# Performance work log

Measured on AMD Instinct MI355X. Metric: run time of the kernel, lower is better.

## Reference

```python
import jax, jax.numpy as jnp
import numpy as np

B, NC, H, W = 8, 384, 32, 32
G, GC = 6, 64            # n_groups, n_group_channels
HEADS, D = 12, 32        # n_heads, n_head_channels
KS, STRIDE = 3, 2
ORF = 2.0                # offset_range_factor
HK = (H - KS) // STRIDE + 1
WK = (W - KS) // STRIDE + 1
NS = HK * WK             # n_sample per branch
NQ = H * W               # query length


def setup_inputs() -> dict:
    key = jax.random.key(0)
    ks = jax.random.split(key, 16)
    def n(k, shape, s=0.02):
        return jax.random.normal(k, shape, jnp.float32) * s
    return {
        "query": jax.random.normal(ks[0], (B, NC, 1, NQ), jnp.float32),
        "x_r1": jax.random.normal(ks[1], (B, NC, H, W), jnp.float32),
        "x_r2": jax.random.normal(ks[2], (B, NC, H, W), jnp.float32),
        "x_x1": jax.random.normal(ks[3], (B, NC, H, W), jnp.float32),
        "x_x2": jax.random.normal(ks[4], (B, NC, H, W), jnp.float32),
        # conv_offset: 1x1 (4gc->gc) + GELU + depthwise kk stride + GELU + 1x1 (gc->2, no bias)
        "off_w1": n(ks[5], (GC, 4 * GC)),
        "off_b1": jnp.zeros((GC,), jnp.float32),
        "off_w2": n(ks[6], (GC, 1, KS, KS), 0.1),
        "off_b2": jnp.zeros((GC,), jnp.float32),
        "off_w3": n(ks[7], (2, GC), 0.1),
        "q_w": n(ks[8], (NC, NC)), "q_b": jnp.zeros((NC,), jnp.float32),
        "k_w": n(ks[9], (NC, NC)), "k_b": jnp.zeros((NC,), jnp.float32),
        "v_w": n(ks[10], (NC, NC)), "v_b": jnp.zeros((NC,), jnp.float32),
        "o_w": n(ks[11], (NC, NC)), "o_b": jnp.zeros((NC,), jnp.float32),
    }


def _conv1x1(x, w, b=None):
    # x: (B, Cin, ...), w: (Cout, Cin)
    y = jnp.einsum('oc,bc...->bo...', w, x)
    if b is not None:
        y = y + b.reshape((1, -1) + (1,) * (y.ndim - 2))
    return y


def _forward(query, x_r1, x_r2, x_x1, x_x2, off_w1, off_b1, off_w2, off_b2,
             off_w3, q_w, q_b, k_w, k_b, v_w, v_b, o_w, o_b):
    gelu = lambda t: jax.nn.gelu(t, approximate=False)
    # shared offset branch: concat 4 maps along channels, split into groups
    data = jnp.concatenate([x_r1, x_r2, x_x1, x_x2], axis=1).reshape(B * G, 4 * GC, H, W)
    t = gelu(_conv1x1(data, off_w1, off_b1))
    t = jax.lax.conv_general_dilated(
        t, off_w2, (STRIDE, STRIDE), 'VALID',
        feature_group_count=GC,
        dimension_numbers=('NCHW', 'OIHW', 'NCHW')) + off_b2[None, :, None, None]
    t = gelu(t)
    offset = _conv1x1(t, off_w3)                      # (BG, 2, HK, WK), ch0=y, ch1=x
    orange = jnp.array([1.0 / (HK - 1.0), 1.0 / (WK - 1.0)], jnp.float32).reshape(1, 2, 1, 1)
    offset = jnp.tanh(offset) * orange * ORF
    offset = offset.transpose(0, 2, 3, 1)             # (BG, HK, WK, 2)
    # reference points (normalized to [-1,1], align_corners=True convention)
    cy = (jnp.arange(HK, dtype=jnp.float32) * STRIDE + KS // 2) / (H - 1.0) * 2.0 - 1.0
    cx = (jnp.arange(WK, dtype=jnp.float32) * STRIDE + KS // 2) / (W - 1.0) * 2.0 - 1.0
    ref = jnp.stack(jnp.meshgrid(cy, cx, indexing='ij'), axis=-1)  # (HK, WK, 2)
    pos = jnp.clip(offset + ref[None], -1.0, 1.0).reshape(B * G, NS, 2)
    gy, gx = pos[..., 0], pos[..., 1]
    # bilinear grid sample, align_corners=True; grid clamped so always in-bounds
    x = (gx + 1.0) * 0.5 * (W - 1)
    y = (gy + 1.0) * 0.5 * (H - 1)
    x0f, y0f = jnp.floor(x), jnp.floor(y)
    wx = (x - x0f)[:, None, :]
    wy = (y - y0f)[:, None, :]
    x0 = jnp.clip(x0f.astype(jnp.int32), 0, W - 1); x1 = jnp.clip(x0 + 1, 0, W - 1)
    y0 = jnp.clip(y0f.astype(jnp.int32), 0, H - 1); y1 = jnp.clip(y0 + 1, 0, H - 1)

    def bsample(img):
        flat = img.reshape(B * G, GC, H * W)
        gat = lambda yi, xi: jnp.take_along_axis(flat, (yi * W + xi)[:, None, :], axis=2)
        out = (gat(y0, x0) * (1 - wy) * (1 - wx) + gat(y0, x1) * (1 - wy) * wx +
               gat(y1, x0) * wy * (1 - wx) + gat(y1, x1) * wy * wx)
        return out.reshape(B, NC, NS)

    sampled = jnp.concatenate(
        [bsample(x_r1), bsample(x_r2), bsample(x_x1), bsample(x_x2)], axis=-1)  # (B, NC, 4*NS)
    q = _conv1x1(query.reshape(B, NC, NQ), q_w, q_b).reshape(B * HEADS, D, NQ)
    k = _conv1x1(sampled, k_w, k_b).reshape(B * HEADS, D, 4 * NS)
    v = _conv1x1(sampled, v_w, v_b).reshape(B * HEADS, D, 4 * NS)
    attn = jax.nn.softmax(jnp.einsum('bcm,bcn->bmn', q, k) * (D ** -0.5), axis=-1)
    out = jnp.einsum('bmn,bcn->bcm', attn, v).reshape(B, NC, NQ)
    out = _conv1x1(out, o_w, o_b)
    return query.reshape(B, NC, NQ) + out  # == out.squeeze(2) of torch


def reference(query, x_r1, x_r2, x_x1, x_x2, off_w1, off_b1, off_w2, off_b2,
              off_w3, q_w, q_b, k_w, k_b, v_w, v_b, o_w, o_b):
    return _forward(query, x_r1, x_r2, x_x1, x_x2, off_w1, off_b1, off_w2,
                    off_b2, off_w3, q_w, q_b, k_w, k_b, v_w, v_b, o_w, o_b)
```

## Files before the change

### kernel.cpp

```cpp
#include <hip/hip_runtime.h>
#include <math.h>

#define Bn 8
#define NCn 384
#define Hn 32
#define Wn 32
#define Gn 6
#define GCn 64
#define HEADSn 12
#define Dn 32
#define HKn 15
#define WKn 15
#define NSn 225
#define NQn 1024
#define NKVn 900
#define VSTRIDE 960

typedef __attribute__((ext_vector_type(8))) short short8;
typedef __attribute__((ext_vector_type(4))) float floatx4;

__device__ __forceinline__ float gelu_f(float x) {
    return 0.5f * x * (1.0f + erff(x * 0.70710678118654752f));
}

__device__ __forceinline__ ushort f2bf(float x) {
    unsigned u = __float_as_uint(x);
    u = (u + 0x7FFF + ((u >> 16) & 1)) >> 16;
    return (ushort)u;
}

__device__ __forceinline__ ushort f2bf_fast(float x) {
    return (ushort)((__float_as_uint(x) + 0x8000u) >> 16);
}

__global__ __launch_bounds__(256) void k_prep(
    const float* __restrict__ xr1, const float* __restrict__ xr2,
    const float* __restrict__ xx1, const float* __restrict__ xx2,
    const float* __restrict__ query,
    const float* __restrict__ w1, const float* __restrict__ qw,
    const float* __restrict__ kw, const float* __restrict__ vw,
    const float* __restrict__ ow,
    ushort* __restrict__ dataT, ushort* __restrict__ qXT,
    ushort* __restrict__ wb)
{
    __shared__ float lds[64 * 65];
    const int id = blockIdx.x;
    const int tid = threadIdx.x;

    if (id < 768) {
        const int bg = id % 48, hwt = id / 48;
        const int b = bg / Gn, g = bg % Gn;
        for (int kc = 0; kc < 4; ++kc) {
            for (int idx = tid; idx < 4096; idx += 256) {
                int cl = idx >> 6, hwl = idx & 63;
                int gch = g * 256 + kc * 64 + cl;
                int m = gch / NCn, cm = gch % NCn;
                const float* img = (m == 0) ? xr1 : (m == 1) ? xr2 : (m == 2) ? xx1 : xx2;
                lds[cl * 65 + hwl] = img[(b * NCn + cm) * NQn + hwt * 64 + hwl];
            }
            __syncthreads();
            for (int idx = tid; idx < 4096; idx += 256) {
                int hwl = idx >> 6, cl = idx & 63;
                dataT[((size_t)bg * NQn + hwt * 64 + hwl) * 256 + kc * 64 + cl] =
                    f2bf(lds[cl * 65 + hwl]);
            }
            __syncthreads();
        }
    } else if (id < 896) {
        const int j = id - 768;
        const int b = j & 7, hwt = j >> 3;
        for (int kc = 0; kc < 6; ++kc) {
            for (int idx = tid; idx < 4096; idx += 256) {
                int cl = idx >> 6, hwl = idx & 63;
                lds[cl * 65 + hwl] =
                    query[((size_t)b * NCn + kc * 64 + cl) * NQn + hwt * 64 + hwl];
            }
            __syncthreads();
            for (int idx = tid; idx < 4096; idx += 256) {
                int hwl = idx >> 6, cl = idx & 63;
                qXT[((size_t)b * NQn + hwt * 64 + hwl) * NCn + kc * 64 + cl] =
                    f2bf(lds[cl * 65 + hwl]);
            }
            __syncthreads();
        }
    } else {
        const int j = id - 896;
        for (int i = j * 256 + tid; i < 606208; i += 128 * 256) {
            float v;
            if      (i < 16384)  v = w1[i];
            else if (i < 163840) v = qw[i - 16384];
            else if (i < 311296) v = kw[i - 163840];
            else if (i < 458752) v = vw[i - 311296];
            else                 v = ow[i - 458752];
            wb[i] = f2bf(v);
        }
    }
}

__global__ __launch_bounds__(256) void k_offsets(
    const float* __restrict__ t1T, const float* __restrict__ w2,
    const float* __restrict__ b2, const float* __restrict__ w3,
    float* __restrict__ posb)
{
    const int wid  = blockIdx.x * 4 + (threadIdx.x >> 6);
    const int lane = threadIdx.x & 63;
    const int bg = wid / NSn, s = wid % NSn;
    const int hk = s / WKn, wk = s % WKn;

    const float* tbase = t1T + ((size_t)bg << 10) * 64;
    const float* wp = w2 + lane * 9;
    float sv = b2[lane];
    #pragma unroll
    for (int i = 0; i < 3; ++i)
        #pragma unroll
        for (int j = 0; j < 3; ++j)
            sv += tbase[(size_t)(((hk * 2 + i) * Wn + wk * 2 + j) * 64 + lane)] * wp[i * 3 + j];
    float gv = gelu_f(sv);
    float ay = w3[lane] * gv;
    float ax = w3[64 + lane] * gv;
    #pragma unroll
    for (int off = 32; off > 0; off >>= 1) {
        ay += __shfl_xor(ay, off, 64);
        ax += __shfl_xor(ax, off, 64);
    }
    if (lane == 0) {
        float fy = tanhf(ay) * (2.0f / 14.0f);
        float fx = tanhf(ax) * (2.0f / 14.0f);
        float cy = (float)(hk * 2 + 1) * (2.0f / 31.0f) - 1.0f;
        float cx = (float)(wk * 2 + 1) * (2.0f / 31.0f) - 1.0f;
        float py = fminf(fmaxf(fy + cy, -1.0f), 1.0f);
        float px = fminf(fmaxf(fx + cx, -1.0f), 1.0f);
        posb[wid * 2 + 0] = (py + 1.0f) * 0.5f * 31.0f;
        posb[wid * 2 + 1] = (px + 1.0f) * 0.5f * 31.0f;
    }
}

__global__ __launch_bounds__(256) void k_sample(
    const float* __restrict__ xr1, const float* __restrict__ xr2,
    const float* __restrict__ xx1, const float* __restrict__ xx2,
    const float* __restrict__ posb, ushort* __restrict__ smpT)
{
    const int b = blockIdx.x & 7;
    const int j = blockIdx.x >> 3;
    const int g = j % Gn, m = j / Gn;
    const int bg = b * Gn + g;
    const int s0 = blockIdx.y * 57;
    const int ns = min(57, NSn - s0);
    const float* img = (m == 0) ? xr1 : (m == 1) ? xr2 : (m == 2) ? xx1 : xx2;

    for (int idx = threadIdx.x; idx < 64 * ns; idx += 256) {
        int c = idx & 63, s = s0 + (idx >> 6);
        float py = posb[(bg * NSn + s) * 2 + 0];
        float px = posb[(bg * NSn + s) * 2 + 1];
        float y0f = floorf(py), x0f = floorf(px);
        float wy = py - y0f, wx = px - x0f;
        int y0 = (int)y0f, x0 = (int)x0f;
        int y1 = min(y0 + 1, Hn - 1), x1 = min(x0 + 1, Wn - 1);
        const float* base = img + (b * NCn + g * GCn + c) * NQn;
        float v00 = base[y0 * Wn + x0], v01 = base[y0 * Wn + x1];
        float v10 = base[y1 * Wn + x0], v11 = base[y1 * Wn + x1];
        float v = v00 * (1.0f - wy) * (1.0f - wx) + v01 * (1.0f - wy) * wx
                + v10 * wy * (1.0f - wx) + v11 * wy * wx;
        smpT[((size_t)b * NQn + m * NSn + s) * NCn + g * GCn + c] = f2bf(v);
    }
}

__global__ __launch_bounds__(256) void k_gemm(
    const ushort* __restrict__ A, const ushort* __restrict__ XT,
    const float* __restrict__ bias, const float* __restrict__ resid,
    float* __restrict__ Yf,
    int K, int Npad, int N, int mode)
{
    const int nb = blockIdx.x, mb = blockIdx.y, b = blockIdx.z;
    const int w = threadIdx.x >> 6, lane = threadIdx.x & 63;
    const int l16 = lane & 15, quad = lane >> 4;
    const int m0 = mb * 32;
    const int n0 = nb * 256 + w * 64;

    floatx4 zero = {0.0f, 0.0f, 0.0f, 0.0f};
    floatx4 acc[2][4] = {{zero, zero, zero, zero}, {zero, zero, zero, zero}};

    const ushort* a0 = A + (size_t)(m0 + l16) * K + quad * 8;
    const ushort* a1 = a0 + (size_t)16 * K;
    const ushort* bp = XT + ((size_t)b * Npad + n0 + l16) * K + quad * 8;

    #pragma unroll 2
    for (int k0 = 0; k0 < K; k0 += 32) {
        short8 af0 = *(const short8*)(a0 + k0);
        short8 af1 = *(const short8*)(a1 + k0);
        short8 bf[4];
        #pragma unroll
        for (int t = 0; t < 4; ++t)
            bf[t] = *(const short8*)(bp + (size_t)(t * 16) * K + k0);
        #pragma unroll
        for (int t = 0; t < 4; ++t) {
            acc[0][t] = __builtin_amdgcn_mfma_f32_16x16x32_bf16(af0, bf[t], acc[0][t], 0, 0, 0);
            acc[1][t] = __builtin_amdgcn_mfma_f32_16x16x32_bf16(af1, bf[t], acc[1][t], 0, 0, 0);
        }
    }

    if (mode == 0) {
        #pragma unroll
        for (int a = 0; a < 2; ++a)
            #pragma unroll
            for (int r = 0; r < 4; ++r) {
                int m = m0 + a * 16 + quad * 4 + r;
                float bb = bias[m];
                #pragma unroll
                for (int t = 0; t < 4; ++t) {
                    int n = n0 + t * 16 + l16;
                    size_t o = ((size_t)b * NCn + m) * N + n;
                    Yf[o] = acc[a][t][r] + bb + resid[o];
                }
            }
    } else {
        #pragma unroll
        for (int a = 0; a < 2; ++a) {
            const int mbase = m0 + a * 16 + quad * 4;
            float bb[4];
            #pragma unroll
            for (int r = 0; r < 4; ++r) bb[r] = bias[mbase + r];
            #pragma unroll
            for (int t = 0; t < 4; ++t) {
                int n = n0 + t * 16 + l16;
                float4 v;
                v.x = gelu_f(acc[a][t][0] + bb[0]);
                v.y = gelu_f(acc[a][t][1] + bb[1]);
                v.z = gelu_f(acc[a][t][2] + bb[2]);
                v.w = gelu_f(acc[a][t][3] + bb[3]);
                *(float4*)&Yf[(((size_t)b << 10) + n) * 64 + mbase] = v;
            }
        }
    }
}

__global__ __launch_bounds__(256) void k_gemm_qkv(
    const ushort* __restrict__ qwb, const ushort* __restrict__ kwb,
    const ushort* __restrict__ vwb,
    const ushort* __restrict__ qXT, const ushort* __restrict__ smpT,
    const float* __restrict__ q_b, const float* __restrict__ k_b,
    const float* __restrict__ v_b,
    ushort* __restrict__ qTb, ushort* __restrict__ kTb, ushort* __restrict__ vTb)
{
    const int nb = blockIdx.x, mb = blockIdx.y;
    const int w = threadIdx.x >> 6, lane = threadIdx.x & 63;
    const int l16 = lane & 15, quad = lane >> 4;
    const int m0 = mb * 32;
    const int n0 = nb * 256 + w * 64;
    const int K = NCn;
    floatx4 zero = {0.0f, 0.0f, 0.0f, 0.0f};

    if (blockIdx.z < Bn) {
        const int b = blockIdx.z;
        floatx4 acc[2][4] = {{zero, zero, zero, zero}, {zero, zero, zero, zero}};
        const ushort* a0 = qwb + (size_t)(m0 + l16) * K + quad * 8;
        const ushort* a1 = a0 + (size_t)16 * K;
        const ushort* bp = qXT + ((size_t)b * NQn + n0 + l16) * K + quad * 8;

        #pragma unroll 2
        for (int k0 = 0; k0 < K; k0 += 32) {
            short8 af0 = *(const short8*)(a0 + k0);
            short8 af1 = *(const short8*)(a1 + k0);
            short8 bf[4];
            #pragma unroll
            for (int t = 0; t < 4; ++t)
                bf[t] = *(const short8*)(bp + (size_t)(t * 16) * K + k0);
            #pragma unroll
            for (int t = 0; t < 4; ++t) {
                acc[0][t] = __builtin_amdgcn_mfma_f32_16x16x32_bf16(af0, bf[t], acc[0][t], 0, 0, 0);
                acc[1][t] = __builtin_amdgcn_mfma_f32_16x16x32_bf16(af1, bf[t], acc[1][t], 0, 0, 0);
            }
        }
        #pragma unroll
        for (int a = 0; a < 2; ++a)
            #pragma unroll
            for (int r = 0; r < 4; ++r) {
                int m = m0 + a * 16 + quad * 4 + r;
                int head = m >> 5, d = m & 31;
                float bb = q_b[m];
                #pragma unroll
                for (int t2 = 0; t2 < 4; ++t2) {
                    int n = n0 + t2 * 16 + l16;
                    qTb[((size_t)(b * HEADSn + head) * NQn + n) * 32 + d] =
                        f2bf(acc[a][t2][r] + bb);
                }
            }
    } else {
        const int b = blockIdx.z - Bn;
        floatx4 acck[2][4] = {{zero, zero, zero, zero}, {zero, zero, zero, zero}};
        floatx4 accv[2][4] = {{zero, zero, zero, zero}, {zero, zero, zero, zero}};
        const ushort* ak0 = kwb + (size_t)(m0 + l16) * K + quad * 8;
        const ushort* av0 = vwb + (size_t)(m0 + l16) * K + quad * 8;
        const ushort* bp  = smpT + ((size_t)b * NQn + n0 + l16) * K + quad * 8;

        for (int k0 = 0; k0 < K; k0 += 32) {
            short8 afk0 = *(const short8*)(ak0 + k0);
            short8 afk1 = *(const short8*)(ak0 + (size_t)16 * K + k0);
            short8 afv0 = *(const short8*)(av0 + k0);
            short8 afv1 = *(const short8*)(av0 + (size_t)16 * K + k0);
            short8 bf[4];
            #pragma unroll
            for (int t = 0; t < 4; ++t)
                bf[t] = *(const short8*)(bp + (size_t)(t * 16) * K + k0);
            #pragma unroll
            for (int t = 0; t < 4; ++t) {
                acck[0][t] = __builtin_amdgcn_mfma_f32_16x16x32_bf16(afk0, bf[t], acck[0][t], 0, 0, 0);
                acck[1][t] = __builtin_amdgcn_mfma_f32_16x16x32_bf16(afk1, bf[t], acck[1][t], 0, 0, 0);
                accv[0][t] = __builtin_amdgcn_mfma_f32_16x16x32_bf16(afv0, bf[t], accv[0][t], 0, 0, 0);
                accv[1][t] = __builtin_amdgcn_mfma_f32_16x16x32_bf16(afv1, bf[t], accv[1][t], 0, 0, 0);
            }
        }
        #pragma unroll
        for (int a = 0; a < 2; ++a)
            #pragma unroll
            for (int r = 0; r < 4; ++r) {
                int m = m0 + a * 16 + quad * 4 + r;
                int head = m >> 5, d = m & 31;
                float bk = k_b[m], bv = v_b[m];
                #pragma unroll
                for (int t2 = 0; t2 < 4; ++t2) {
                    int n = n0 + t2 * 16 + l16;
                    if (n < NKVn)
                        kTb[((size_t)(b * HEADSn + head) * NKVn + n) * 32 + d] =
                            f2bf(acck[a][t2][r] + bk);
                    if (n < VSTRIDE)
                        vTb[((size_t)b * NCn + m) * VSTRIDE + n] =
                            (n < NKVn) ? f2bf(accv[a][t2][r] + bv) : (ushort)0;
                }
            }
    }
}

__global__ __launch_bounds__(256) void k_attn_mfma(
    const ushort* __restrict__ qT, const ushort* __restrict__ kT,
    const ushort* __restrict__ vb, ushort* __restrict__ aoutT)
{
    __shared__ __align__(16) ushort p_lds[4 * 2 * 16 * 80];
    const int b = blockIdx.x & 7;
    const int j = blockIdx.x >> 3;
    const int h = j % HEADSn, mt = j / HEADSn;
    const int bh = b * HEADSn + h;
    const int tid = threadIdx.x;
    const int w = tid >> 6, lane = tid & 63;
    const int l16 = lane & 15, quad = lane >> 4;
    const float cexp = 0.25503486f;

    ushort* p_w[2] = { p_lds + (w * 2 + 0) * (16 * 80),
                       p_lds + (w * 2 + 1) * (16 * 80) };

    const int q0 = mt * 128 + w * 32;
    short8 qf[2];
    qf[0] = *(const short8*)(qT + (size_t)((bh * NQn + q0 + l16) * 32 + quad * 8));
    qf[1] = *(const short8*)(qT + (size_t)((bh * NQn + q0 + 16 + l16) * 32 + quad * 8));

    const ushort* kbase = kT + (size_t)bh * NKVn * 32;
    const ushort* vbase = vb + ((size_t)b * NCn + h * Dn) * VSTRIDE;

    floatx4 zero = {0.0f, 0.0f, 0.0f, 0.0f};
    floatx4 oacc[2][2] = {{zero, zero}, {zero, zero}};
    float lrun[2][4] = {};

    short8 kf[4];
    #pragma unroll
    for (int t = 0; t < 4; ++t)
        kf[t] = *(const short8*)(kbase + (size_t)((t * 16 + l16) * 32 + quad * 8));

    for (int nc = 0; nc < 15; ++nc) {
        const int n0 = nc * 64;
        short8 vf[2][2];
        #pragma unroll
        for (int kc = 0; kc < 2; ++kc)
            #pragma unroll
            for (int nt2 = 0; nt2 < 2; ++nt2)
                vf[kc][nt2] = *(const short8*)(vbase +
                    (size_t)((nt2 * 16 + l16) * VSTRIDE + n0 + kc * 32 + quad * 8));

        floatx4 sf[2][4];
        #pragma unroll
        for (int a = 0; a < 2; ++a)
            #pragma unroll
            for (int t = 0; t < 4; ++t)
                sf[a][t] = __builtin_amdgcn_mfma_f32_16x16x32_bf16(qf[a], kf[t], zero, 0, 0, 0);

        if (nc < 14) {
            #pragma unroll
            for (int t = 0; t < 4; ++t)
                kf[t] = *(const short8*)(kbase +
                    (size_t)((n0 + 64 + t * 16 + l16) * 32 + quad * 8));
        }

        if (n0 + 64 <= NKVn) {
            #pragma unroll
            for (int a = 0; a < 2; ++a)
                #pragma unroll
                for (int t = 0; t < 4; ++t)
                    #pragma unroll
                    for (int r = 0; r < 4; ++r) {
                        float p = exp2f(sf[a][t][r] * cexp);
                        lrun[a][r] += p;
                        p_w[a][(quad * 4 + r) * 80 + t * 16 + l16] = f2bf_fast(p);
                    }
        } else {
            const int limit = NKVn - n0;
            #pragma unroll
            for (int a = 0; a < 2; ++a)
                #pragma unroll
                for (int t = 0; t < 4; ++t) {
                    const int col = t * 16 + l16;
                    #pragma unroll
                    for (int r = 0; r < 4; ++r) {
                        float p = (col < limit) ? exp2f(sf[a][t][r] * cexp) : 0.0f;
                        lrun[a][r] += p;
                        p_w[a][(quad * 4 + r) * 80 + col] = f2bf_fast(p);
                    }
                }
        }

        #pragma unroll
        for (int a = 0; a < 2; ++a)
            #pragma unroll
            for (int kc = 0; kc < 2; ++kc) {
                const short8 pf = *(const short8*)(p_w[a] + l16 * 80 + kc * 32 + quad * 8);
                #pragma unroll
                for (int nt2 = 0; nt2 < 2; ++nt2)
                    oacc[a][nt2] = __builtin_amdgcn_mfma_f32_16x16x32_bf16(
                        pf, vf[kc][nt2], oacc[a][nt2], 0, 0, 0);
            }
    }

    #pragma unroll
    for (int a = 0; a < 2; ++a)
        #pragma unroll
        for (int r = 0; r < 4; ++r) {
            float l = lrun[a][r];
            l += __shfl_xor(l, 1, 64);
            l += __shfl_xor(l, 2, 64);
            l += __shfl_xor(l, 4, 64);
            l += __shfl_xor(l, 8, 64);
            lrun[a][r] = 1.0f / l;
        }

    #pragma unroll
    for (int a = 0; a < 2; ++a)
        #pragma unroll
        for (int nt2 = 0; nt2 < 2; ++nt2)
            #pragma unroll
            for (int r = 0; r < 4; ++r) {
                int m = q0 + a * 16 + quad * 4 + r;
                int d = h * Dn + nt2 * 16 + l16;
                aoutT[((size_t)b * NQn + m) * NCn + d] =
                    f2bf(oacc[a][nt2][r] * lrun[a][r]);
            }
}

extern "C" void kernel_launch(void* const* d_in, const int* in_sizes, int n_in,
                              void* d_out, int out_size, void* d_ws, size_t ws_size,
                              hipStream_t stream) {
    const float* query = (const float*)d_in[0];
    const float* xr1   = (const float*)d_in[1];
    const float* xr2   = (const float*)d_in[2];
    const float* xx1   = (const float*)d_in[3];
    const float* xx2   = (const float*)d_in[4];
    const float* w1    = (const float*)d_in[5];
    const float* b1    = (const float*)d_in[6];
    const float* w2    = (const float*)d_in[7];
    const float* b2    = (const float*)d_in[8];
    const float* w3    = (const float*)d_in[9];
    const float* q_w   = (const float*)d_in[10];
    const float* q_b   = (const float*)d_in[11];
    const float* k_w   = (const float*)d_in[12];
    const float* k_b   = (const float*)d_in[13];
    const float* v_w   = (const float*)d_in[14];
    const float* v_b   = (const float*)d_in[15];
    const float* o_w   = (const float*)d_in[16];
    const float* o_b   = (const float*)d_in[17];
    float* out = (float*)d_out;

    float* ws = (float*)d_ws;
    ushort* dataT = (ushort*)ws;
    ushort* qTb   = (ushort*)(ws + 1572864);
    ushort* aoutT = (ushort*)(ws + 3145728);
    float*  t1T   = ws + 6291456;
    ushort* kTb   = (ushort*)(ws + 6291456);
    ushort* vTb   = (ushort*)(ws + 7673856);
    float*  posb  = ws + 9437184;
    ushort* smpT  = (ushort*)(ws + 9458816);
    ushort* wb    = (ushort*)(ws + 11031680);
    ushort* w1b = wb;
    ushort* qwb = wb + 16384;
    ushort* kwb = wb + 163840;
    ushort* vwb = wb + 311296;
    ushort* owb = wb + 458752;
    ushort* qXT2 = wb + 606208;

    k_prep<<<dim3(1024), 256, 0, stream>>>(xr1, xr2, xx1, xx2, query,
                                           w1, q_w, k_w, v_w, o_w,
                                           dataT, qXT2, wb);
    k_gemm<<<dim3(4, 2, 48), 256, 0, stream>>>(w1b, dataT, b1, nullptr,
                                               t1T, 256, NQn, NQn, 3);
    k_offsets<<<dim3(2700), 256, 0, stream>>>(t1T, w2, b2, w3, posb);
    k_sample<<<dim3(192, 4), 256, 0, stream>>>(xr1, xr2, xx1, xx2, posb, smpT);
    k_gemm_qkv<<<dim3(4, 12, 16), 256, 0, stream>>>(qwb, kwb, vwb, qXT2, smpT,
                                                    q_b, k_b, v_b, qTb, kTb, vTb);
    k_attn_mfma<<<dim3(768), 256, 0, stream>>>(qTb, kTb, vTb, aoutT);
    k_gemm<<<dim3(4, 12, Bn), 256, 0, stream>>>(owb, aoutT, o_b, query,
                                                out, NCn, NQn, NQn, 0);
}
```

Measured before the change: 300.5 us.

## Block K dimension into 32-wide panels for QKV GEMM operands and vectorize stores

```diff
diff --git a/kernel.cpp b/kernel.cpp
--- a/kernel.cpp
+++ b/kernel.cpp
@@ -15,6 +15,7 @@
 #define NQn 1024
 #define NKVn 900
 #define VSTRIDE 960
+#define KBq 12
 
 typedef __attribute__((ext_vector_type(8))) short short8;
 typedef __attribute__((ext_vector_type(4))) float floatx4;
@@ -78,7 +79,9 @@
             __syncthreads();
             for (int idx = tid; idx < 4096; idx += 256) {
                 int hwl = idx >> 6, cl = idx & 63;
-                qXT[((size_t)b * NQn + hwt * 64 + hwl) * NCn + kc * 64 + cl] =
+                int ch = kc * 64 + cl;
+                int kb = ch >> 5, k32 = ch & 31;
+                qXT[((size_t)(b * KBq + kb) * NQn + hwt * 64 + hwl) * 32 + k32] =
                     f2bf(lds[cl * 65 + hwl]);
             }
             __syncthreads();
@@ -87,11 +90,20 @@
         const int j = id - 896;
         for (int i = j * 256 + tid; i < 606208; i += 128 * 256) {
             float v;
-            if      (i < 16384)  v = w1[i];
-            else if (i < 163840) v = qw[i - 16384];
-            else if (i < 311296) v = kw[i - 163840];
-            else if (i < 458752) v = vw[i - 311296];
-            else                 v = ow[i - 458752];
+            if (i < 16384) {
+                v = w1[i];
+            } else if (i < 163840) {
+                int t = i - 16384, kb = t / 12288, r = t % 12288;
+                v = qw[(r >> 5) * NCn + kb * 32 + (r & 31)];
+            } else if (i < 311296) {
+                int t = i - 163840, kb = t / 12288, r = t % 12288;
+                v = kw[(r >> 5) * NCn + kb * 32 + (r & 31)];
+            } else if (i < 458752) {
+                int t = i - 311296, kb = t / 12288, r = t % 12288;
+                v = vw[(r >> 5) * NCn + kb * 32 + (r & 31)];
+            } else {
+                v = ow[i - 458752];
+            }
             wb[i] = f2bf(v);
         }
     }
@@ -161,7 +173,10 @@
         float v10 = base[y1 * Wn + x0], v11 = base[y1 * Wn + x1];
         float v = v00 * (1.0f - wy) * (1.0f - wx) + v01 * (1.0f - wy) * wx
                 + v10 * wy * (1.0f - wx) + v11 * wy * wx;
-        smpT[((size_t)b * NQn + m * NSn + s) * NCn + g * GCn + c] = f2bf(v);
+        int ch = g * GCn + c;
+        int kb = ch >> 5, k32 = ch & 31;
+        int n = m * NSn + s;
+        smpT[((size_t)(b * KBq + kb) * NQn + n) * 32 + k32] = f2bf(v);
     }
 }
 
@@ -247,24 +262,24 @@
     const int l16 = lane & 15, quad = lane >> 4;
     const int m0 = mb * 32;
     const int n0 = nb * 256 + w * 64;
-    const int K = NCn;
     floatx4 zero = {0.0f, 0.0f, 0.0f, 0.0f};
 
     if (blockIdx.z < Bn) {
         const int b = blockIdx.z;
         floatx4 acc[2][4] = {{zero, zero, zero, zero}, {zero, zero, zero, zero}};
-        const ushort* a0 = qwb + (size_t)(m0 + l16) * K + quad * 8;
-        const ushort* a1 = a0 + (size_t)16 * K;
-        const ushort* bp = qXT + ((size_t)b * NQn + n0 + l16) * K + quad * 8;
+        const ushort* a0 = qwb + (size_t)(m0 + l16) * 32 + quad * 8;
+        const ushort* bp = qXT + ((size_t)b * KBq * NQn + n0 + l16) * 32 + quad * 8;
 
         #pragma unroll 2
-        for (int k0 = 0; k0 < K; k0 += 32) {
-            short8 af0 = *(const short8*)(a0 + k0);
-            short8 af1 = *(const short8*)(a1 + k0);
+        for (int kb = 0; kb < KBq; ++kb) {
+            const ushort* ak = a0 + (size_t)kb * (NCn * 32);
+            const ushort* bk = bp + (size_t)kb * (NQn * 32);
+            short8 af0 = *(const short8*)(ak);
+            short8 af1 = *(const short8*)(ak + 16 * 32);
             short8 bf[4];
             #pragma unroll
             for (int t = 0; t < 4; ++t)
-                bf[t] = *(const short8*)(bp + (size_t)(t * 16) * K + k0);
+                bf[t] = *(const short8*)(bk + t * 16 * 32);
             #pragma unroll
             for (int t = 0; t < 4; ++t) {
                 acc[0][t] = __builtin_amdgcn_mfma_f32_16x16x32_bf16(af0, bf[t], acc[0][t], 0, 0, 0);
@@ -272,36 +287,39 @@
             }
         }
         #pragma unroll
-        for (int a = 0; a < 2; ++a)
-            #pragma unroll
-            for (int r = 0; r < 4; ++r) {
-                int m = m0 + a * 16 + quad * 4 + r;
-                int head = m >> 5, d = m & 31;
-                float bb = q_b[m];
-                #pragma unroll
-                for (int t2 = 0; t2 < 4; ++t2) {
-                    int n = n0 + t2 * 16 + l16;
-                    qTb[((size_t)(b * HEADSn + head) * NQn + n) * 32 + d] =
-                        f2bf(acc[a][t2][r] + bb);
-                }
-            }
+        for (int a = 0; a < 2; ++a) {
+            #pragma unroll
+            for (int t2 = 0; t2 < 4; ++t2) {
+                int n = n0 + t2 * 16 + l16;
+                ushort4 pk;
+                pk.x = f2bf(acc[a][t2][0] + q_b[m0 + a * 16 + quad * 4 + 0]);
+                pk.y = f2bf(acc[a][t2][1] + q_b[m0 + a * 16 + quad * 4 + 1]);
+                pk.z = f2bf(acc[a][t2][2] + q_b[m0 + a * 16 + quad * 4 + 2]);
+                pk.w = f2bf(acc[a][t2][3] + q_b[m0 + a * 16 + quad * 4 + 3]);
+                *(ushort4*)&qTb[((size_t)(b * HEADSn + mb) * NQn + n) * 32 +
+                                a * 16 + quad * 4] = pk;
+            }
+        }
     } else {
         const int b = blockIdx.z - Bn;
         floatx4 acck[2][4] = {{zero, zero, zero, zero}, {zero, zero, zero, zero}};
         floatx4 accv[2][4] = {{zero, zero, zero, zero}, {zero, zero, zero, zero}};
-        const ushort* ak0 = kwb + (size_t)(m0 + l16) * K + quad * 8;
-        const ushort* av0 = vwb + (size_t)(m0 + l16) * K + quad * 8;
-        const ushort* bp  = smpT + ((size_t)b * NQn + n0 + l16) * K + quad * 8;
-
-        for (int k0 = 0; k0 < K; k0 += 32) {
-            short8 afk0 = *(const short8*)(ak0 + k0);
-            short8 afk1 = *(const short8*)(ak0 + (size_t)16 * K + k0);
-            short8 afv0 = *(const short8*)(av0 + k0);
-            short8 afv1 = *(const short8*)(av0 + (size_t)16 * K + k0);
+        const ushort* ak0 = kwb + (size_t)(m0 + l16) * 32 + quad * 8;
+        const ushort* av0 = vwb + (size_t)(m0 + l16) * 32 + quad * 8;
+        const ushort* bp  = smpT + ((size_t)b * KBq * NQn + n0 + l16) * 32 + quad * 8;
+
+        for (int kb = 0; kb < KBq; ++kb) {
+            const ushort* ak = ak0 + (size_t)kb * (NCn * 32);
+            const ushort* av = av0 + (size_t)kb * (NCn * 32);
+            const ushort* bk = bp + (size_t)kb * (NQn * 32);
+            short8 afk0 = *(const short8*)(ak);
+            short8 afk1 = *(const short8*)(ak + 16 * 32);
+            short8 afv0 = *(const short8*)(av);
+            short8 afv1 = *(const short8*)(av + 16 * 32);
             short8 bf[4];
             #pragma unroll
             for (int t = 0; t < 4; ++t)
-                bf[t] = *(const short8*)(bp + (size_t)(t * 16) * K + k0);
+                bf[t] = *(const short8*)(bk + t * 16 * 32);
             #pragma unroll
             for (int t = 0; t < 4; ++t) {
                 acck[0][t] = __builtin_amdgcn_mfma_f32_16x16x32_bf16(afk0, bf[t], acck[0][t], 0, 0, 0);
@@ -311,18 +329,30 @@
             }
         }
         #pragma unroll
+        for (int a = 0; a < 2; ++a) {
+            #pragma unroll
+            for (int t2 = 0; t2 < 4; ++t2) {
+                int n = n0 + t2 * 16 + l16;
+                if (n < NKVn) {
+                    ushort4 pk;
+                    pk.x = f2bf(acck[a][t2][0] + k_b[m0 + a * 16 + quad * 4 + 0]);
+                    pk.y = f2bf(acck[a][t2][1] + k_b[m0 + a * 16 + quad * 4 + 1]);
+                    pk.z = f2bf(acck[a][t2][2] + k_b[m0 + a * 16 + quad * 4 + 2]);
+                    pk.w = f2bf(acck[a][t2][3] + k_b[m0 + a * 16 + quad * 4 + 3]);
+                    *(ushort4*)&kTb[((size_t)(b * HEADSn + mb) * NKVn + n) * 32 +
+                                    a * 16 + quad * 4] = pk;
+                }
+            }
+        }
+        #pragma unroll
         for (int a = 0; a < 2; ++a)
             #pragma unroll
             for (int r = 0; r < 4; ++r) {
                 int m = m0 + a * 16 + quad * 4 + r;
-                int head = m >> 5, d = m & 31;
-                float bk = k_b[m], bv = v_b[m];
+                float bv = v_b[m];
                 #pragma unroll
                 for (int t2 = 0; t2 < 4; ++t2) {
                     int n = n0 + t2 * 16 + l16;
-                    if (n < NKVn)
-                        kTb[((size_t)(b * HEADSn + head) * NKVn + n) * 32 + d] =
-                            f2bf(acck[a][t2][r] + bk);
                     if (n < VSTRIDE)
                         vTb[((size_t)b * NCn + m) * VSTRIDE + n] =
                             (n < NKVn) ? f2bf(accv[a][t2][r] + bv) : (ushort)0;
```

Measured after the change: 289.2 us. 3.8% less time.
